# Performance work log

Measured on AMD Instinct MI355X. Metric: run time of the kernel, lower is better.

Reference implementation:

```python
import jax, jax.numpy as jnp
import numpy as np

NEG_INF = -1e30

def setup_inputs() -> dict:
    key = jax.random.key(0)
    ks = jax.random.split(key, 8)
    N, E = 4096, 16384
    Fn, Fe, Dn, De = 128, 64, 128, 64
    # xavier_uniform bound = sqrt(6/(fan_in+fan_out)); for 1-D params torch treats shape as (1, len)
    bn = np.sqrt(6.0 / (Fn + Dn))
    be = np.sqrt(6.0 / (Fe + De))
    return {
        "node_features": jax.random.normal(ks[0], (N, Fn), dtype=jnp.float32),
        "edge_features": jax.random.normal(ks[1], (E, Fe), dtype=jnp.float32),
        "adjacency_matrix": jax.random.randint(ks[2], (N, N), 0, 2, dtype=jnp.int32),
        "edge_adjacency_matrix": jax.random.randint(ks[3], (E, N), 0, 2, dtype=jnp.int32),
        "weight_node": jax.random.uniform(ks[4], (Fn, Dn), minval=-bn, maxval=bn, dtype=jnp.float32),
        "weight_edge": jax.random.uniform(ks[5], (Fe, De), minval=-be, maxval=be, dtype=jnp.float32),
        "parameter_vector_node": jax.random.uniform(ks[6], (2 * Dn,), minval=-1.0, maxval=1.0, dtype=jnp.float32),
        "parameter_vector_edge": jax.random.uniform(ks[7], (Dn + De,), minval=-1.0, maxval=1.0, dtype=jnp.float32),
    }


def reference(node_features, edge_features, adjacency_matrix, edge_adjacency_matrix,
              weight_node, weight_edge, parameter_vector_node, parameter_vector_edge):
    lrelu = jax.nn.leaky_relu  # default negative_slope=0.01, matches torch LeakyReLU
    Dn = weight_node.shape[1]

    h = node_features @ weight_node          # [N, Dn]
    he = edge_features @ weight_edge         # [E, De]

    # ---- node-level attention ----
    a_self, a_neigh = parameter_vector_node[:Dn], parameter_vector_node[Dn:]
    # score[i, j] = leaky_relu(a . cat(h_i, h_j)) for j a neighbor of i (adjacency[j, i] > 0)
    s_n = lrelu((h @ a_self)[:, None] + (h @ a_neigh)[None, :])   # [N, N]
    mask_n = adjacency_matrix.T > 0                                # [N, N], row i = neighbors of i
    coef_n = jax.nn.softmax(jnp.where(mask_n, s_n, NEG_INF), axis=1)
    coef_n = jnp.where(mask_n, coef_n, 0.0)
    deg_n = jnp.sum(mask_n, axis=1).astype(h.dtype)                # [N]
    means_n = (coef_n @ node_features) / deg_n[:, None]            # [N, Fn] (torch.mean divides by deg)
    out_n = lrelu(means_n @ weight_node)                           # [N, Dn]

    # ---- edge-level attention ----
    b_self, b_edge = parameter_vector_edge[:Dn], parameter_vector_edge[Dn:]
    s_e = lrelu((h @ b_self)[:, None] + (he @ b_edge)[None, :])    # [N, E]
    mask_e = edge_adjacency_matrix.T > 0                           # [N, E]
    coef_e = jax.nn.softmax(jnp.where(mask_e, s_e, NEG_INF), axis=1)
    coef_e = jnp.where(mask_e, coef_e, 0.0)
    deg_e = jnp.sum(mask_e, axis=1).astype(h.dtype)
    means_e = (coef_e @ edge_features) / deg_e[:, None]            # [N, Fe]
    out_e = lrelu(means_e @ weight_edge)                           # [N, De]

    return jnp.concatenate([out_n, out_e], axis=1)                 # [N, Dn+De]
```

## Files before the change

### kernel.cpp

```cpp
#include <hip/hip_runtime.h>

typedef short bf16x8 __attribute__((ext_vector_type(8)));
typedef float f32x4 __attribute__((ext_vector_type(4)));

#define N_NODES 4096
#define N_EDGES 16384
#define FN 128
#define FE 64
#define NJS 8
#define EJS 16

__device__ __forceinline__ float lrelu(float x) { return x >= 0.f ? x : 0.01f * x; }
__device__ __forceinline__ unsigned short f2bf(float f) {
    unsigned int x = __float_as_uint(f);
    return (unsigned short)((x + 0x7fffu + ((x >> 16) & 1u)) >> 16);
}

__global__ __launch_bounds__(256) void k_node_proj(
    const float* __restrict__ nf, const float* __restrict__ Wn,
    const float* __restrict__ pvn, const float* __restrict__ pve,
    float* __restrict__ alpha, float* __restrict__ beta, float* __restrict__ gamma) {
    __shared__ float row[4][FN];
    const int wv = threadIdx.x >> 6, ln = threadIdx.x & 63;
    const int i = blockIdx.x * 4 + wv;
    float2 r2 = *(const float2*)(nf + (size_t)i * FN + ln * 2);
    row[wv][ln * 2] = r2.x; row[wv][ln * 2 + 1] = r2.y;
    __syncthreads();
    float h0 = 0.f, h1 = 0.f;
#pragma unroll 8
    for (int k = 0; k < FN; ++k) {
        float nv = row[wv][k];
        float2 w2 = *(const float2*)(Wn + (size_t)k * FN + ln * 2);
        h0 = fmaf(nv, w2.x, h0); h1 = fmaf(nv, w2.y, h1);
    }
    float2 as = *(const float2*)(pvn + ln * 2);
    float2 an = *(const float2*)(pvn + FN + ln * 2);
    float2 bs = *(const float2*)(pve + ln * 2);
    float pa = h0 * as.x + h1 * as.y;
    float pb = h0 * an.x + h1 * an.y;
    float pg = h0 * bs.x + h1 * bs.y;
#pragma unroll
    for (int off = 32; off > 0; off >>= 1) {
        pa += __shfl_down(pa, off, 64);
        pb += __shfl_down(pb, off, 64);
        pg += __shfl_down(pg, off, 64);
    }
    if (ln == 0) { alpha[i] = pa; beta[i] = pb; gamma[i] = pg; }
}

__global__ __launch_bounds__(256) void k_edge_proj(
    const float* __restrict__ ef, const float* __restrict__ We,
    const float* __restrict__ pve, float* __restrict__ betaE) {
    __shared__ float row[4][FE];
    const int wv = threadIdx.x >> 6, ln = threadIdx.x & 63;
    const int e = blockIdx.x * 4 + wv;
    row[wv][ln] = ef[(size_t)e * FE + ln];
    __syncthreads();
    float h = 0.f;
#pragma unroll 8
    for (int k = 0; k < FE; ++k)
        h = fmaf(row[wv][k], We[(size_t)k * FE + ln], h);
    float p = h * pve[FN + ln];
#pragma unroll
    for (int off = 32; off > 0; off >>= 1) p += __shfl_down(p, off, 64);
    if (ln == 0) betaE[e] = p;
}

__global__ __launch_bounds__(256) void k_maxes(
    const float* __restrict__ beta, const float* __restrict__ betaE,
    float* __restrict__ maxes) {
    const float* src = blockIdx.x == 0 ? beta : betaE;
    const int n = blockIdx.x == 0 ? N_NODES : N_EDGES;
    float m = -3.0e38f;
    for (int t = threadIdx.x; t < n; t += 256) m = fmaxf(m, src[t]);
#pragma unroll
    for (int off = 32; off > 0; off >>= 1) m = fmaxf(m, __shfl_down(m, off, 64));
    __shared__ float sm[4];
    if ((threadIdx.x & 63) == 0) sm[threadIdx.x >> 6] = m;
    __syncthreads();
    if (threadIdx.x == 0)
        maxes[blockIdx.x] = fmaxf(fmaxf(sm[0], sm[1]), fmaxf(sm[2], sm[3]));
}

__global__ __launch_bounds__(256) void k_prep(
    const float* __restrict__ src, unsigned short* __restrict__ dst,
    const int J, const int F) {
    __shared__ float tile[64][65];
    const int t = threadIdx.x;
    const int j0 = blockIdx.x * 64, f0 = blockIdx.y * 64;
#pragma unroll
    for (int p = 0; p < 4; ++p) {
        int j = (t >> 4) + p * 16;
        float4 v = *(const float4*)(src + (size_t)(j0 + j) * F + f0 + (t & 15) * 4);
        tile[j][(t & 15) * 4 + 0] = v.x;
        tile[j][(t & 15) * 4 + 1] = v.y;
        tile[j][(t & 15) * 4 + 2] = v.z;
        tile[j][(t & 15) * 4 + 3] = v.w;
    }
    __syncthreads();
#pragma unroll
    for (int p = 0; p < 2; ++p) {
        int f = (t >> 3) + p * 32;
        int c = t & 7;
        bf16x8 v;
#pragma unroll
        for (int e = 0; e < 8; ++e) v[e] = (short)f2bf(tile[c * 8 + e][f]);
        *(bf16x8*)(dst + (size_t)(f0 + f) * J + j0 + c * 8) = v;
    }
}

__global__ __launch_bounds__(256) void k_node_att(
    const unsigned short* __restrict__ Xt,
    const int* __restrict__ adj,
    const float* __restrict__ alpha, const float* __restrict__ beta,
    const float* __restrict__ maxes,
    float* __restrict__ accP, float* __restrict__ zP, float* __restrict__ degP) {
    __shared__ unsigned short xlds[2][128 * 64];
    __shared__ unsigned short wlds[2][4 * 512];
    __shared__ float bb[512];
    __shared__ float zred[8][32];
    __shared__ float dred[8][32];
    const int t = threadIdx.x;
    const int i0 = blockIdx.x * 32;
    const int bj = blockIdx.y;
    const int j0 = bj * (N_NODES / NJS);
    const int il = t & 31;
    const int jg = t >> 5;
    const float a_i = alpha[i0 + il];
    const float m_i = lrelu(a_i + maxes[0]);
    if (t < 128) *(float4*)&bb[t * 4] = *(const float4*)(beta + j0 + t * 4);
    const int l = t & 63, wid = t >> 6;
    const int wm = wid >> 1, wn = wid & 1;
    const int l15 = l & 15, l4 = l >> 4;
    const int sf = t >> 3, sc = t & 7;
    const int xswz = (sc ^ (sf & 7)) * 8;
    const int wdst = ((jg >> 2) * 2 + (il >> 4)) * 512 + ((il & 15) + 16 * (jg & 3)) * 8;
    f32x4 acc[4] = {{0,0,0,0},{0,0,0,0},{0,0,0,0},{0,0,0,0}};
    float zacc = 0.f, dacc = 0.f;

    const int* mp0 = adj + (size_t)(j0 + jg * 8) * N_NODES + i0 + il;
    const unsigned short* xs0 = Xt + (size_t)sf * N_NODES + j0 + sc * 8;

    int mk[8];
#pragma unroll
    for (int e = 0; e < 8; ++e) mk[e] = mp0[(size_t)e * N_NODES];
    bf16x8 xv0 = *(const bf16x8*)(xs0);
    bf16x8 xv1 = *(const bf16x8*)(xs0 + (size_t)32 * N_NODES);
    bf16x8 xv2 = *(const bf16x8*)(xs0 + (size_t)64 * N_NODES);
    bf16x8 xv3 = *(const bf16x8*)(xs0 + (size_t)96 * N_NODES);
    __syncthreads();

    int buf = 0;
    for (int ks = 0; ks < 8; ++ks) {
        const int jb = ks * 64;
        bf16x8 wfrag;
#pragma unroll
        for (int e = 0; e < 8; ++e) {
            float s = lrelu(a_i + bb[jb + jg * 8 + e]);
            float w = mk[e] > 0 ? __expf(s - m_i) : 0.f;
            zacc += w;
            dacc += (float)mk[e];
            wfrag[e] = (short)f2bf(w);
        }
        *(bf16x8*)&xlds[buf][(sf +  0) * 64 + xswz] = xv0;
        *(bf16x8*)&xlds[buf][(sf + 32) * 64 + xswz] = xv1;
        *(bf16x8*)&xlds[buf][(sf + 64) * 64 + xswz] = xv2;
        *(bf16x8*)&xlds[buf][(sf + 96) * 64 + xswz] = xv3;
        *(bf16x8*)&wlds[buf][wdst] = wfrag;
        if (ks + 1 < 8) {
            const int jbn = jb + 64;
            const int* mp = mp0 + (size_t)jbn * N_NODES;
#pragma unroll
            for (int e = 0; e < 8; ++e) mk[e] = mp[(size_t)e * N_NODES];
            const unsigned short* xs = xs0 + jbn;
            xv0 = *(const bf16x8*)(xs);
            xv1 = *(const bf16x8*)(xs + (size_t)32 * N_NODES);
            xv2 = *(const bf16x8*)(xs + (size_t)64 * N_NODES);
            xv3 = *(const bf16x8*)(xs + (size_t)96 * N_NODES);
        }
        __syncthreads();
#pragma unroll
        for (int kb = 0; kb < 2; ++kb) {
            bf16x8 b = *(const bf16x8*)&wlds[buf][(kb * 2 + wn) * 512 + l * 8];
#pragma unroll
            for (int mi = 0; mi < 4; ++mi) {
                const int fr = wm * 64 + mi * 16 + l15;
                bf16x8 a = *(const bf16x8*)&xlds[buf][fr * 64 + (((kb * 4 + l4) ^ (fr & 7)) * 8)];
                acc[mi] = __builtin_amdgcn_mfma_f32_16x16x32_bf16(a, b, acc[mi], 0, 0, 0);
            }
        }
        buf ^= 1;
    }
    zred[jg][il] = zacc;
    dred[jg][il] = dacc;
    __syncthreads();
    if (t < 32) {
        float z = 0.f, d = 0.f;
#pragma unroll
        for (int g = 0; g < 8; ++g) { z += zred[g][t]; d += dred[g][t]; }
        zP[bj * N_NODES + i0 + t] = z;
        degP[bj * N_NODES + i0 + t] = d;
    }
    const int ig = i0 + wn * 16 + l15;
#pragma unroll
    for (int mi = 0; mi < 4; ++mi) {
        const int fg = wm * 64 + mi * 16 + l4 * 4;
        *(f32x4*)(accP + ((size_t)bj * N_NODES + ig) * FN + fg) = acc[mi];
    }
}

__global__ __launch_bounds__(256) void k_edge_att(
    const unsigned short* __restrict__ Xt,
    const int* __restrict__ eadj,
    const float* __restrict__ gamma, const float* __restrict__ betaE,
    const float* __restrict__ maxes,
    float* __restrict__ accP, float* __restrict__ zP, float* __restrict__ degP) {
    __shared__ unsigned short xlds[2][64 * 64];
    __shared__ unsigned short wlds[2][8 * 512];
    __shared__ float bb[1024];
    __shared__ float zred[4][64];
    __shared__ float dred[4][64];
    const int t = threadIdx.x;
    const int i0 = blockIdx.x * 64;
    const int bj = blockIdx.y;
    const int j0 = bj * (N_EDGES / EJS);
    const int il = t & 63;
    const int jg = t >> 6;
    const float g_i = gamma[i0 + il];
    const float m_i = lrelu(g_i + maxes[1]);
    *(float4*)&bb[t * 4] = *(const float4*)(betaE + j0 + t * 4);
    const int l = t & 63, wid = t >> 6;
    const int wm = wid >> 1, wn = wid & 1;
    const int l15 = l & 15, l4 = l >> 4;
    const int sf = t >> 2, sc = t & 3;
    const int xd0 = sf * 64 + ((sc       ^ (sf & 7)) * 8);
    const int xd1 = sf * 64 + (((sc + 4) ^ (sf & 7)) * 8);
    const unsigned short* xsrc = Xt + (size_t)sf * N_EDGES + j0 + sc * 8;
    const int wl = (il & 15) + 16 * jg;
    const int nb = il >> 4;
    f32x4 acc[2][2] = {{{0,0,0,0},{0,0,0,0}},{{0,0,0,0},{0,0,0,0}}};
    float zacc = 0.f, dacc = 0.f;

    const int* mp0 = eadj + (size_t)(j0 + jg * 8) * N_NODES + i0 + il;

    int mk0[8], mk1[8];
#pragma unroll
    for (int e = 0; e < 8; ++e) mk0[e] = mp0[(size_t)e * N_NODES];
#pragma unroll
    for (int e = 0; e < 8; ++e) mk1[e] = mp0[(size_t)(32 + e) * N_NODES];
    bf16x8 xv0 = *(const bf16x8*)(xsrc);
    bf16x8 xv1 = *(const bf16x8*)(xsrc + 32);
    __syncthreads();

    int buf = 0;
    for (int ks = 0; ks < 16; ++ks) {
        const int jb = ks * 64;
        bf16x8 wf0, wf1;
#pragma unroll
        for (int e = 0; e < 8; ++e) {
            float s0 = lrelu(g_i + bb[jb + jg * 8 + e]);
            float w0 = mk0[e] > 0 ? __expf(s0 - m_i) : 0.f;
            float s1 = lrelu(g_i + bb[jb + 32 + jg * 8 + e]);
            float w1 = mk1[e] > 0 ? __expf(s1 - m_i) : 0.f;
            zacc += w0 + w1;
            dacc += (float)(mk0[e] + mk1[e]);
            wf0[e] = (short)f2bf(w0);
            wf1[e] = (short)f2bf(w1);
        }
        *(bf16x8*)&xlds[buf][xd0] = xv0;
        *(bf16x8*)&xlds[buf][xd1] = xv1;
        *(bf16x8*)&wlds[buf][(0 * 4 + nb) * 512 + wl * 8] = wf0;
        *(bf16x8*)&wlds[buf][(1 * 4 + nb) * 512 + wl * 8] = wf1;
        if (ks + 1 < 16) {
            const int jbn = jb + 64;
            const int* mp = mp0 + (size_t)jbn * N_NODES;
#pragma unroll
            for (int e = 0; e < 8; ++e) mk0[e] = mp[(size_t)e * N_NODES];
#pragma unroll
            for (int e = 0; e < 8; ++e) mk1[e] = mp[(size_t)(32 + e) * N_NODES];
            xv0 = *(const bf16x8*)(xsrc + jbn);
            xv1 = *(const bf16x8*)(xsrc + jbn + 32);
        }
        __syncthreads();
#pragma unroll
        for (int kb = 0; kb < 2; ++kb) {
            bf16x8 b0 = *(const bf16x8*)&wlds[buf][(kb * 4 + wn * 2 + 0) * 512 + l * 8];
            bf16x8 b1 = *(const bf16x8*)&wlds[buf][(kb * 4 + wn * 2 + 1) * 512 + l * 8];
#pragma unroll
            for (int mi = 0; mi < 2; ++mi) {
                const int fr = wm * 32 + mi * 16 + l15;
                bf16x8 a = *(const bf16x8*)&xlds[buf][fr * 64 + (((kb * 4 + l4) ^ (fr & 7)) * 8)];
                acc[mi][0] = __builtin_amdgcn_mfma_f32_16x16x32_bf16(a, b0, acc[mi][0], 0, 0, 0);
                acc[mi][1] = __builtin_amdgcn_mfma_f32_16x16x32_bf16(a, b1, acc[mi][1], 0, 0, 0);
            }
        }
        buf ^= 1;
    }
    zred[jg][il] = zacc;
    dred[jg][il] = dacc;
    __syncthreads();
    if (t < 64) {
        float z = zred[0][t] + zred[1][t] + zred[2][t] + zred[3][t];
        float d = dred[0][t] + dred[1][t] + dred[2][t] + dred[3][t];
        zP[bj * N_NODES + i0 + t] = z;
        degP[bj * N_NODES + i0 + t] = d;
    }
    const size_t obase = (size_t)bj * N_NODES;
#pragma unroll
    for (int mi = 0; mi < 2; ++mi) {
#pragma unroll
        for (int p = 0; p < 2; ++p) {
            int ig = i0 + wn * 32 + p * 16 + l15;
            int fg = wm * 32 + mi * 16 + l4 * 4;
            *(f32x4*)(accP + (obase + ig) * FE + fg) = acc[mi][p];
        }
    }
}

__global__ __launch_bounds__(256) void k_node_out(
    const float* __restrict__ accP, const float* __restrict__ zP,
    const float* __restrict__ degP, const float* __restrict__ Wn,
    float* __restrict__ out) {
    __shared__ float ml[4][FN];
    const int wv = threadIdx.x >> 6, ln = threadIdx.x & 63;
    const int i = blockIdx.x * 4 + wv;
    float s0 = 0.f, s1 = 0.f;
#pragma unroll
    for (int js = 0; js < NJS; ++js) {
        float2 v = *(const float2*)(accP + ((size_t)js * N_NODES + i) * FN + ln * 2);
        s0 += v.x; s1 += v.y;
    }
    float z = 0.f, d = 0.f;
#pragma unroll
    for (int js = 0; js < NJS; ++js) { z += zP[js * N_NODES + i]; d += degP[js * N_NODES + i]; }
    float zd = z * d;
    float inv = zd > 0.f ? 1.f / zd : 0.f;
    ml[wv][ln * 2] = s0 * inv; ml[wv][ln * 2 + 1] = s1 * inv;
    __syncthreads();
    float o0 = 0.f, o1 = 0.f;
#pragma unroll 8
    for (int k = 0; k < FN; ++k) {
        float mvv = ml[wv][k];
        float2 w2 = *(const float2*)(Wn + (size_t)k * FN + ln * 2);
        o0 = fmaf(mvv, w2.x, o0); o1 = fmaf(mvv, w2.y, o1);
    }
    out[(size_t)i * 192 + ln * 2] = lrelu(o0);
    out[(size_t)i * 192 + ln * 2 + 1] = lrelu(o1);
}

__global__ __launch_bounds__(256) void k_edge_out(
    const float* __restrict__ accP, const float* __restrict__ zP,
    const float* __restrict__ degP, const float* __restrict__ We,
    float* __restrict__ out) {
    __shared__ float ml[4][FE];
    const int wv = threadIdx.x >> 6, ln = threadIdx.x & 63;
    const int i = blockIdx.x * 4 + wv;
    float s = 0.f;
#pragma unroll
    for (int js = 0; js < EJS; ++js)
        s += accP[((size_t)js * N_NODES + i) * FE + ln];
    float z = 0.f, d = 0.f;
#pragma unroll
    for (int js = 0; js < EJS; ++js) { z += zP[js * N_NODES + i]; d += degP[js * N_NODES + i]; }
    float zd = z * d;
    float inv = zd > 0.f ? 1.f / zd : 0.f;
    ml[wv][ln] = s * inv;
    __syncthreads();
    float o = 0.f;
#pragma unroll 8
    for (int k = 0; k < FE; ++k)
        o = fmaf(ml[wv][k], We[(size_t)k * FE + ln], o);
    out[(size_t)i * 192 + 128 + ln] = lrelu(o);
}

extern "C" void kernel_launch(void* const* d_in, const int* in_sizes, int n_in,
                              void* d_out, int out_size, void* d_ws, size_t ws_size,
                              hipStream_t stream) {
    (void)in_sizes; (void)n_in; (void)out_size; (void)ws_size;
    const float* nf   = (const float*)d_in[0];
    const float* ef   = (const float*)d_in[1];
    const int*   adj  = (const int*)d_in[2];
    const int*   eadj = (const int*)d_in[3];
    const float* Wn   = (const float*)d_in[4];
    const float* We   = (const float*)d_in[5];
    const float* pvn  = (const float*)d_in[6];
    const float* pve  = (const float*)d_in[7];
    float* out = (float*)d_out;

    float* alpha = (float*)d_ws;
    float* beta  = alpha + 4096;
    float* gamma = beta + 4096;
    float* betaE = gamma + 4096;
    float* maxes = betaE + 16384;
    unsigned short* XtN = (unsigned short*)(maxes + 64);
    unsigned short* XtE = XtN + (size_t)FN * N_NODES;
    float* accN = (float*)(XtE + (size_t)FE * N_EDGES);
    float* zN   = accN + (size_t)NJS * N_NODES * FN;
    float* degN = zN + (size_t)NJS * N_NODES;
    float* accE = degN + (size_t)NJS * N_NODES;
    float* zE   = accE + (size_t)EJS * N_NODES * FE;
    float* degE = zE + (size_t)EJS * N_NODES;

    k_node_proj<<<N_NODES / 4, 256, 0, stream>>>(nf, Wn, pvn, pve, alpha, beta, gamma);
    k_edge_proj<<<N_EDGES / 4, 256, 0, stream>>>(ef, We, pve, betaE);
    k_maxes<<<2, 256, 0, stream>>>(beta, betaE, maxes);
    k_prep<<<dim3(N_NODES / 64, FN / 64), 256, 0, stream>>>(nf, XtN, N_NODES, FN);
    k_prep<<<dim3(N_EDGES / 64, FE / 64), 256, 0, stream>>>(ef, XtE, N_EDGES, FE);
    k_node_att<<<dim3(N_NODES / 32, NJS), 256, 0, stream>>>(XtN, adj, alpha, beta, maxes, accN, zN, degN);
    k_edge_att<<<dim3(N_NODES / 64, EJS), 256, 0, stream>>>(XtE, eadj, gamma, betaE, maxes, accE, zE, degE);
    k_node_out<<<N_NODES / 4, 256, 0, stream>>>(accN, zN, degN, Wn, out);
    k_edge_out<<<N_NODES / 4, 256, 0, stream>>>(accE, zE, degE, We, out);
}
```

Baseline: 165.1 us.

## Pack adjacency matrices into bitmasks before attention kernels

Adds a streaming pre-pass that turns the int32 node and edge adjacency matrices into 64-bit ballot bitmasks. The attention kernels then read one bit per element from the packed words instead of strided int32 loads. The aim is to move the heavy mask traffic into a simple, bandwidth-friendly kernel and cut memory latency inside the MFMA loops. The full int32 matrices are still read once, and the change adds one kernel launch plus workspace for the bitmasks.

```diff
diff --git a/kernel.cpp b/kernel.cpp
--- a/kernel.cpp
+++ b/kernel.cpp
@@ -2,6 +2,7 @@
 
 typedef short bf16x8 __attribute__((ext_vector_type(8)));
 typedef float f32x4 __attribute__((ext_vector_type(4)));
+typedef unsigned long long u64;
 
 #define N_NODES 4096
 #define N_EDGES 16384
@@ -9,11 +10,37 @@
 #define FE 64
 #define NJS 8
 #define EJS 16
+#define WPR 64
 
 __device__ __forceinline__ float lrelu(float x) { return x >= 0.f ? x : 0.01f * x; }
 __device__ __forceinline__ unsigned short f2bf(float f) {
     unsigned int x = __float_as_uint(f);
     return (unsigned short)((x + 0x7fffu + ((x >> 16) & 1u)) >> 16);
+}
+
+__global__ __launch_bounds__(256) void k_pack(
+    const int* __restrict__ adj, const int* __restrict__ eadj,
+    u64* __restrict__ adjP, u64* __restrict__ eadjP) {
+    const int wv = threadIdx.x >> 6, ln = threadIdx.x & 63;
+    const int row = blockIdx.x * 4 + wv;
+    const int* src;
+    u64* dst;
+    if (row < N_EDGES) {
+        src = eadj + (size_t)row * N_NODES;
+        dst = eadjP + (size_t)row * WPR;
+    } else {
+        src = adj + (size_t)(row - N_EDGES) * N_NODES;
+        dst = adjP + (size_t)(row - N_EDGES) * WPR;
+    }
+#pragma unroll 4
+    for (int chunk = 0; chunk < 16; ++chunk) {
+        int4 v = *(const int4*)(src + chunk * 256 + ln * 4);
+        u64 b0 = __ballot(v.x > 0);
+        u64 b1 = __ballot(v.y > 0);
+        u64 b2 = __ballot(v.z > 0);
+        u64 b3 = __ballot(v.w > 0);
+        if (ln < 4) dst[chunk * 4 + ln] = (ln == 0) ? b0 : (ln == 1) ? b1 : (ln == 2) ? b2 : b3;
+    }
 }
 
 __global__ __launch_bounds__(256) void k_node_proj(
@@ -111,7 +138,7 @@
 
 __global__ __launch_bounds__(256) void k_node_att(
     const unsigned short* __restrict__ Xt,
-    const int* __restrict__ adj,
+    const u64* __restrict__ adjP,
     const float* __restrict__ alpha, const float* __restrict__ beta,
     const float* __restrict__ maxes,
     float* __restrict__ accP, float* __restrict__ zP, float* __restrict__ degP) {
@@ -138,12 +165,13 @@
     f32x4 acc[4] = {{0,0,0,0},{0,0,0,0},{0,0,0,0},{0,0,0,0}};
     float zacc = 0.f, dacc = 0.f;
 
-    const int* mp0 = adj + (size_t)(j0 + jg * 8) * N_NODES + i0 + il;
+    const u64* mp0 = adjP + (size_t)(j0 + jg * 8) * WPR + ((i0 >> 8) * 4 + (il & 3));
+    const int mbit = ((i0 + il) >> 2) & 63;
     const unsigned short* xs0 = Xt + (size_t)sf * N_NODES + j0 + sc * 8;
 
     int mk[8];
 #pragma unroll
-    for (int e = 0; e < 8; ++e) mk[e] = mp0[(size_t)e * N_NODES];
+    for (int e = 0; e < 8; ++e) mk[e] = (int)((mp0[(size_t)e * WPR] >> mbit) & 1);
     bf16x8 xv0 = *(const bf16x8*)(xs0);
     bf16x8 xv1 = *(const bf16x8*)(xs0 + (size_t)32 * N_NODES);
     bf16x8 xv2 = *(const bf16x8*)(xs0 + (size_t)64 * N_NODES);
@@ -157,7 +185,7 @@
 #pragma unroll
         for (int e = 0; e < 8; ++e) {
             float s = lrelu(a_i + bb[jb + jg * 8 + e]);
-            float w = mk[e] > 0 ? __expf(s - m_i) : 0.f;
+            float w = mk[e] ? __expf(s - m_i) : 0.f;
             zacc += w;
             dacc += (float)mk[e];
             wfrag[e] = (short)f2bf(w);
@@ -169,9 +197,9 @@
         *(bf16x8*)&wlds[buf][wdst] = wfrag;
         if (ks + 1 < 8) {
             const int jbn = jb + 64;
-            const int* mp = mp0 + (size_t)jbn * N_NODES;
-#pragma unroll
-            for (int e = 0; e < 8; ++e) mk[e] = mp[(size_t)e * N_NODES];
+            const u64* mp = mp0 + (size_t)jbn * WPR;
+#pragma unroll
+            for (int e = 0; e < 8; ++e) mk[e] = (int)((mp[(size_t)e * WPR] >> mbit) & 1);
             const unsigned short* xs = xs0 + jbn;
             xv0 = *(const bf16x8*)(xs);
             xv1 = *(const bf16x8*)(xs + (size_t)32 * N_NODES);
@@ -211,7 +239,7 @@
 
 __global__ __launch_bounds__(256) void k_edge_att(
     const unsigned short* __restrict__ Xt,
-    const int* __restrict__ eadj,
+    const u64* __restrict__ eadjP,
     const float* __restrict__ gamma, const float* __restrict__ betaE,
     const float* __restrict__ maxes,
     float* __restrict__ accP, float* __restrict__ zP, float* __restrict__ degP) {
@@ -241,13 +269,14 @@
     f32x4 acc[2][2] = {{{0,0,0,0},{0,0,0,0}},{{0,0,0,0},{0,0,0,0}}};
     float zacc = 0.f, dacc = 0.f;
 
-    const int* mp0 = eadj + (size_t)(j0 + jg * 8) * N_NODES + i0 + il;
+    const u64* mp0 = eadjP + (size_t)(j0 + jg * 8) * WPR + ((i0 >> 8) * 4 + (il & 3));
+    const int mbit = ((i0 + il) >> 2) & 63;
 
     int mk0[8], mk1[8];
 #pragma unroll
-    for (int e = 0; e < 8; ++e) mk0[e] = mp0[(size_t)e * N_NODES];
-#pragma unroll
-    for (int e = 0; e < 8; ++e) mk1[e] = mp0[(size_t)(32 + e) * N_NODES];
+    for (int e = 0; e < 8; ++e) mk0[e] = (int)((mp0[(size_t)e * WPR] >> mbit) & 1);
+#pragma unroll
+    for (int e = 0; e < 8; ++e) mk1[e] = (int)((mp0[(size_t)(32 + e) * WPR] >> mbit) & 1);
     bf16x8 xv0 = *(const bf16x8*)(xsrc);
     bf16x8 xv1 = *(const bf16x8*)(xsrc + 32);
     __syncthreads();
@@ -259,9 +288,9 @@
 #pragma unroll
         for (int e = 0; e < 8; ++e) {
             float s0 = lrelu(g_i + bb[jb + jg * 8 + e]);
-            float w0 = mk0[e] > 0 ? __expf(s0 - m_i) : 0.f;
+            float w0 = mk0[e] ? __expf(s0 - m_i) : 0.f;
             float s1 = lrelu(g_i + bb[jb + 32 + jg * 8 + e]);
-            float w1 = mk1[e] > 0 ? __expf(s1 - m_i) : 0.f;
+            float w1 = mk1[e] ? __expf(s1 - m_i) : 0.f;
             zacc += w0 + w1;
             dacc += (float)(mk0[e] + mk1[e]);
             wf0[e] = (short)f2bf(w0);
@@ -273,11 +302,11 @@
         *(bf16x8*)&wlds[buf][(1 * 4 + nb) * 512 + wl * 8] = wf1;
         if (ks + 1 < 16) {
             const int jbn = jb + 64;
-            const int* mp = mp0 + (size_t)jbn * N_NODES;
-#pragma unroll
-            for (int e = 0; e < 8; ++e) mk0[e] = mp[(size_t)e * N_NODES];
-#pragma unroll
-            for (int e = 0; e < 8; ++e) mk1[e] = mp[(size_t)(32 + e) * N_NODES];
+            const u64* mp = mp0 + (size_t)jbn * WPR;
+#pragma unroll
+            for (int e = 0; e < 8; ++e) mk0[e] = (int)((mp[(size_t)e * WPR] >> mbit) & 1);
+#pragma unroll
+            for (int e = 0; e < 8; ++e) mk1[e] = (int)((mp[(size_t)(32 + e) * WPR] >> mbit) & 1);
             xv0 = *(const bf16x8*)(xsrc + jbn);
             xv1 = *(const bf16x8*)(xsrc + jbn + 32);
         }
@@ -387,7 +416,9 @@
     const float* pve  = (const float*)d_in[7];
     float* out = (float*)d_out;
 
-    float* alpha = (float*)d_ws;
+    u64* adjP  = (u64*)d_ws;
+    u64* eadjP = adjP + (size_t)N_NODES * WPR;
+    float* alpha = (float*)(eadjP + (size_t)N_EDGES * WPR);
     float* beta  = alpha + 4096;
     float* gamma = beta + 4096;
     float* betaE = gamma + 4096;
@@ -401,13 +432,14 @@
     float* zE   = accE + (size_t)EJS * N_NODES * FE;
     float* degE = zE + (size_t)EJS * N_NODES;
 
+    k_pack<<<(N_NODES + N_EDGES) / 4, 256, 0, stream>>>(adj, eadj, adjP, eadjP);
     k_node_proj<<<N_NODES / 4, 256, 0, stream>>>(nf, Wn, pvn, pve, alpha, beta, gamma);
     k_edge_proj<<<N_EDGES / 4, 256, 0, stream>>>(ef, We, pve, betaE);
     k_maxes<<<2, 256, 0, stream>>>(beta, betaE, maxes);
     k_prep<<<dim3(N_NODES / 64, FN / 64), 256, 0, stream>>>(nf, XtN, N_NODES, FN);
     k_prep<<<dim3(N_EDGES / 64, FE / 64), 256, 0, stream>>>(ef, XtE, N_EDGES, FE);
-    k_node_att<<<dim3(N_NODES / 32, NJS), 256, 0, stream>>>(XtN, adj, alpha, beta, maxes, accN, zN, degN);
-    k_edge_att<<<dim3(N_NODES / 64, EJS), 256, 0, stream>>>(XtE, eadj, gamma, betaE, maxes, accE, zE, degE);
+    k_node_att<<<dim3(N_NODES / 32, NJS), 256, 0, stream>>>(XtN, adjP, alpha, beta, maxes, accN, zN, degN);
+    k_edge_att<<<dim3(N_NODES / 64, EJS), 256, 0, stream>>>(XtE, eadjP, gamma, betaE, maxes, accE, zE, degE);
     k_node_out<<<N_NODES / 4, 256, 0, stream>>>(accN, zN, degN, Wn, out);
     k_edge_out<<<N_NODES / 4, 256, 0, stream>>>(accE, zE, degE, We, out);
 }
```

Result: slower. 225.4 us (+36.6%).
